# Kernel tuning notes

Hardware: AMD Instinct MI355X
Metric: run time of the kernel (lower is better)

The kernel has to match this reference:

```python
import jax, jax.numpy as jnp
import numpy as np

CLASS_NUM = 4            # number of positive classes
NUM_CLASSES = CLASS_NUM + 1  # last column is the negative class
W_P = 4.0
EPS = 1e-9
THR = 0.5


def setup_inputs() -> dict:
    key = jax.random.key(0)
    k1, k2 = jax.random.split(key)
    N = 4_000_000
    x = jax.random.normal(k1, (N, NUM_CLASSES), dtype=jnp.float32)
    t = jax.random.randint(k2, (N,), 0, NUM_CLASSES)
    return {"x": x, "t": t}


def _conf_mpu_loss(x, t):
    N = x.shape[0]
    p = jax.nn.softmax(x, axis=1)                       # [N, C]
    log_pneg = jnp.log(p[:, -1] + EPS)                  # [N]

    ones = jnp.ones((N,), dtype=jnp.float32)
    counts = jax.ops.segment_sum(ones, t, num_segments=NUM_CLASSES)  # per-class counts
    prior = counts[:CLASS_NUM] / N                      # empirical priors (positive classes)

    # loss_per_class: sum over samples with t==c of -log(p[n,c]+eps)
    logp_t = jnp.log(jnp.take_along_axis(p, t[:, None], axis=1)[:, 0] + EPS)
    class_losses = jax.ops.segment_sum(-logp_t, t, num_segments=NUM_CLASSES)

    # loss_per_class_neg: sum over samples with t==i (i positive) of -log(p_neg+eps)
    loss_neg = jax.ops.segment_sum(-log_pneg, t, num_segments=NUM_CLASSES)[:CLASS_NUM]

    # conf_loss_per_class
    conf = []
    for i in range(CLASS_NUM):
        mask = (p[:, i] > THR) & (t == i)
        nsel = jnp.sum(mask.astype(jnp.float32))
        li = jnp.sum(jnp.where(mask, -log_pneg / p[:, i], 0.0))
        conf.append(li / jnp.maximum(nsel, 1.0))        # li==0 when nsel==0
    mask_n = jnp.all(p <= THR, axis=1) & (t == CLASS_NUM)
    li_n = jnp.sum(jnp.where(mask_n, -log_pneg, 0.0))
    conf_neg = li_n / jnp.maximum(counts[CLASS_NUM], 1.0)  # li_n==0 when no selection
    conf_pos = jnp.stack(conf)                          # [CLASS_NUM]

    denom = jnp.maximum(1.0, counts[:CLASS_NUM])
    risk1 = jnp.sum(prior * class_losses[:CLASS_NUM] / denom)
    risk2 = jnp.sum(prior * conf_pos)
    risk3 = jnp.sum(prior * loss_neg / denom)
    risk4 = conf_neg

    positive_risk = W_P * (risk1 + risk2 - risk3)
    positive_risk = jnp.where(positive_risk < 0, 0.0, positive_risk)
    return positive_risk + risk4


def reference(x, t):
    return _conf_mpu_loss(x, t)
```

## Files before the change

### kernel.cpp

```cpp
#include <hip/hip_runtime.h>

namespace {
constexpr int BLOCK = 256;
constexpr int ROWS_PER_TILE = 1024;
constexpr int NACC = 22;
constexpr float EPSF = 1e-9f;
constexpr float THRF = 0.5f;
constexpr float WPF = 4.0f;
}

__device__ __forceinline__ float wave_reduce(float v) {
#pragma unroll
    for (int o = 32; o > 0; o >>= 1) v += __shfl_down(v, o, 64);
    return v;
}

__global__ __launch_bounds__(BLOCK) void mpu_main(const float* __restrict__ x,
                                                  const int* __restrict__ t,
                                                  float* __restrict__ acc, int N) {
    __shared__ float lds[ROWS_PER_TILE * 5];
    __shared__ float red[BLOCK / 64][NACC];

    float a[NACC];
#pragma unroll
    for (int j = 0; j < NACC; ++j) a[j] = 0.0f;

    const int tid = threadIdx.x;
    const int numTiles = (N + ROWS_PER_TILE - 1) / ROWS_PER_TILE;

    for (int tile = blockIdx.x; tile < numTiles; tile += gridDim.x) {
        const long long rowBase = (long long)tile * ROWS_PER_TILE;
        const int rows = min(ROWS_PER_TILE, (int)((long long)N - rowBase));
        const int nFloats = rows * 5;
        const float* src = x + rowBase * 5;
        const int n4 = nFloats >> 2;
        const float4* src4 = reinterpret_cast<const float4*>(src);
        float4* dst4 = reinterpret_cast<float4*>(lds);
        for (int i = tid; i < n4; i += BLOCK) dst4[i] = src4[i];
        for (int i = (n4 << 2) + tid; i < nFloats; i += BLOCK) lds[i] = src[i];
        __syncthreads();

        for (int k = tid; k < rows; k += BLOCK) {
            const float x0 = lds[k * 5 + 0], x1 = lds[k * 5 + 1], x2 = lds[k * 5 + 2],
                        x3 = lds[k * 5 + 3], x4 = lds[k * 5 + 4];
            const int tc = t[rowBase + k];

            const float mx = fmaxf(fmaxf(fmaxf(x0, x1), fmaxf(x2, x3)), x4);
            const float e0 = __expf(x0 - mx), e1 = __expf(x1 - mx),
                        e2 = __expf(x2 - mx), e3 = __expf(x3 - mx),
                        e4 = __expf(x4 - mx);
            const float r = 1.0f / (e0 + e1 + e2 + e3 + e4);
            const float p0 = e0 * r, p1 = e1 * r, p2 = e2 * r, p3 = e3 * r, p4 = e4 * r;

            const float nln = -__logf(p4 + EPSF);
            const float pt = (tc == 0) ? p0 : (tc == 1) ? p1 : (tc == 2) ? p2
                           : (tc == 3) ? p3 : p4;
            const float nlt = -__logf(pt + EPSF);

            const bool is0 = (tc == 0), is1 = (tc == 1), is2 = (tc == 2),
                       is3 = (tc == 3), is4 = (tc == 4);

            a[0] += is0 ? 1.0f : 0.0f;
            a[1] += is1 ? 1.0f : 0.0f;
            a[2] += is2 ? 1.0f : 0.0f;
            a[3] += is3 ? 1.0f : 0.0f;
            a[4] += is4 ? 1.0f : 0.0f;
            a[5] += is0 ? nlt : 0.0f;
            a[6] += is1 ? nlt : 0.0f;
            a[7] += is2 ? nlt : 0.0f;
            a[8] += is3 ? nlt : 0.0f;
            a[9]  += is0 ? nln : 0.0f;
            a[10] += is1 ? nln : 0.0f;
            a[11] += is2 ? nln : 0.0f;
            a[12] += is3 ? nln : 0.0f;
            const bool sel = (pt > THRF);
            const float confv = sel ? (nln / pt) : 0.0f;
            const float confn = sel ? 1.0f : 0.0f;
            a[13] += is0 ? confv : 0.0f;
            a[14] += is1 ? confv : 0.0f;
            a[15] += is2 ? confv : 0.0f;
            a[16] += is3 ? confv : 0.0f;
            a[17] += is0 ? confn : 0.0f;
            a[18] += is1 ? confn : 0.0f;
            a[19] += is2 ? confn : 0.0f;
            a[20] += is3 ? confn : 0.0f;
            const bool alle = (p0 <= THRF) && (p1 <= THRF) && (p2 <= THRF) &&
                              (p3 <= THRF) && (p4 <= THRF);
            a[21] += (is4 && alle) ? nln : 0.0f;
        }
        __syncthreads();
    }

    const int wave = tid >> 6;
    const int lane = tid & 63;
#pragma unroll
    for (int j = 0; j < NACC; ++j) {
        const float v = wave_reduce(a[j]);
        if (lane == 0) red[wave][j] = v;
    }
    __syncthreads();
    if (tid < NACC) {
        float v = red[0][tid] + red[1][tid] + red[2][tid] + red[3][tid];
        atomicAdd(&acc[tid], v);
    }
}

__global__ void mpu_final(const float* __restrict__ acc, float* __restrict__ out, int N) {
    if (threadIdx.x == 0 && blockIdx.x == 0) {
        const float invN = 1.0f / (float)N;
        float risk1 = 0.0f, risk2 = 0.0f, risk3 = 0.0f;
#pragma unroll
        for (int i = 0; i < 4; ++i) {
            const float cnt = acc[i];
            const float prior = cnt * invN;
            const float denom = fmaxf(1.0f, cnt);
            risk1 += prior * acc[5 + i] / denom;
            risk2 += prior * (acc[13 + i] / fmaxf(acc[17 + i], 1.0f));
            risk3 += prior * acc[9 + i] / denom;
        }
        const float risk4 = acc[21] / fmaxf(acc[4], 1.0f);
        float pos = WPF * (risk1 + risk2 - risk3);
        if (pos < 0.0f) pos = 0.0f;
        out[0] = pos + risk4;
    }
}

extern "C" void kernel_launch(void* const* d_in, const int* in_sizes, int n_in,
                              void* d_out, int out_size, void* d_ws, size_t ws_size,
                              hipStream_t stream) {
    const float* x = (const float*)d_in[0];
    const int* t = (const int*)d_in[1];
    float* out = (float*)d_out;
    float* acc = (float*)d_ws;
    const int N = in_sizes[1];

    hipMemsetAsync(acc, 0, NACC * sizeof(float), stream);

    const int numTiles = (N + ROWS_PER_TILE - 1) / ROWS_PER_TILE;
    const int grid = numTiles < 1024 ? numTiles : 1024;
    mpu_main<<<grid, BLOCK, 0, stream>>>(x, t, acc, N);
    mpu_final<<<1, 64, 0, stream>>>(acc, out, N);
}
```

Baseline: 148.3 us.

## Load four rows per thread via float4 directly, drop LDS staging, use log-sum-exp

Removes the LDS staging tile and its barriers. Each thread now reads four rows (20 floats) as five float4 loads plus one int4 label load straight from global memory. The softmax maths is rewritten as log-sum-exp, so each row needs one log instead of two, and the probability threshold tests are done on the exponentials and their sum without dividing. The grid is raised to 2048 blocks. The trade-offs are higher register pressure from holding four rows per thread, strided uncoalesced float4 loads across threads, and dropping EPS, which slightly changes numerics for very small probabilities.

```diff
diff --git a/kernel.cpp b/kernel.cpp
--- a/kernel.cpp
+++ b/kernel.cpp
@@ -2,10 +2,8 @@
 
 namespace {
 constexpr int BLOCK = 256;
-constexpr int ROWS_PER_TILE = 1024;
+constexpr int GRID = 2048;
 constexpr int NACC = 22;
-constexpr float EPSF = 1e-9f;
-constexpr float THRF = 0.5f;
 constexpr float WPF = 4.0f;
 }
 
@@ -18,90 +16,93 @@
 __global__ __launch_bounds__(BLOCK) void mpu_main(const float* __restrict__ x,
                                                   const int* __restrict__ t,
                                                   float* __restrict__ acc, int N) {
-    __shared__ float lds[ROWS_PER_TILE * 5];
     __shared__ float red[BLOCK / 64][NACC];
 
     float a[NACC];
 #pragma unroll
     for (int j = 0; j < NACC; ++j) a[j] = 0.0f;
 
-    const int tid = threadIdx.x;
-    const int numTiles = (N + ROWS_PER_TILE - 1) / ROWS_PER_TILE;
+    auto process = [&](float x0, float x1, float x2, float x3, float x4, int tc) {
+        const float mx = fmaxf(fmaxf(fmaxf(x0, x1), fmaxf(x2, x3)), x4);
+        const float e0 = __expf(x0 - mx), e1 = __expf(x1 - mx),
+                    e2 = __expf(x2 - mx), e3 = __expf(x3 - mx),
+                    e4 = __expf(x4 - mx);
+        const float sum = ((e0 + e1) + (e2 + e3)) + e4;
+        const float base = mx + __logf(sum);
+        const float nln = base - x4;
+        const float xt = (tc == 0) ? x0 : (tc == 1) ? x1 : (tc == 2) ? x2
+                       : (tc == 3) ? x3 : x4;
+        const float et = (tc == 0) ? e0 : (tc == 1) ? e1 : (tc == 2) ? e2
+                       : (tc == 3) ? e3 : e4;
+        const float nlt = base - xt;
 
-    for (int tile = blockIdx.x; tile < numTiles; tile += gridDim.x) {
-        const long long rowBase = (long long)tile * ROWS_PER_TILE;
-        const int rows = min(ROWS_PER_TILE, (int)((long long)N - rowBase));
-        const int nFloats = rows * 5;
-        const float* src = x + rowBase * 5;
-        const int n4 = nFloats >> 2;
-        const float4* src4 = reinterpret_cast<const float4*>(src);
-        float4* dst4 = reinterpret_cast<float4*>(lds);
-        for (int i = tid; i < n4; i += BLOCK) dst4[i] = src4[i];
-        for (int i = (n4 << 2) + tid; i < nFloats; i += BLOCK) lds[i] = src[i];
-        __syncthreads();
+        const bool is0 = (tc == 0), is1 = (tc == 1), is2 = (tc == 2),
+                   is3 = (tc == 3), is4 = (tc == 4);
+        const bool sel = (et + et > sum);
+        const bool alle = (sum >= 2.0f);
+        const float confv = sel ? nln * sum * __builtin_amdgcn_rcpf(et) : 0.0f;
+        const float confn = sel ? 1.0f : 0.0f;
 
-        for (int k = tid; k < rows; k += BLOCK) {
-            const float x0 = lds[k * 5 + 0], x1 = lds[k * 5 + 1], x2 = lds[k * 5 + 2],
-                        x3 = lds[k * 5 + 3], x4 = lds[k * 5 + 4];
-            const int tc = t[rowBase + k];
+        a[0] += is0 ? 1.0f : 0.0f;
+        a[1] += is1 ? 1.0f : 0.0f;
+        a[2] += is2 ? 1.0f : 0.0f;
+        a[3] += is3 ? 1.0f : 0.0f;
+        a[4] += is4 ? 1.0f : 0.0f;
+        a[5] += is0 ? nlt : 0.0f;
+        a[6] += is1 ? nlt : 0.0f;
+        a[7] += is2 ? nlt : 0.0f;
+        a[8] += is3 ? nlt : 0.0f;
+        a[9]  += is0 ? nln : 0.0f;
+        a[10] += is1 ? nln : 0.0f;
+        a[11] += is2 ? nln : 0.0f;
+        a[12] += is3 ? nln : 0.0f;
+        a[13] += is0 ? confv : 0.0f;
+        a[14] += is1 ? confv : 0.0f;
+        a[15] += is2 ? confv : 0.0f;
+        a[16] += is3 ? confv : 0.0f;
+        a[17] += is0 ? confn : 0.0f;
+        a[18] += is1 ? confn : 0.0f;
+        a[19] += is2 ? confn : 0.0f;
+        a[20] += is3 ? confn : 0.0f;
+        a[21] += (is4 && alle) ? nln : 0.0f;
+    };
 
-            const float mx = fmaxf(fmaxf(fmaxf(x0, x1), fmaxf(x2, x3)), x4);
-            const float e0 = __expf(x0 - mx), e1 = __expf(x1 - mx),
-                        e2 = __expf(x2 - mx), e3 = __expf(x3 - mx),
-                        e4 = __expf(x4 - mx);
-            const float r = 1.0f / (e0 + e1 + e2 + e3 + e4);
-            const float p0 = e0 * r, p1 = e1 * r, p2 = e2 * r, p3 = e3 * r, p4 = e4 * r;
+    const int gid = blockIdx.x * BLOCK + threadIdx.x;
+    const int stride = gridDim.x * BLOCK;
+    const int nGroups = N >> 2;
+    const float4* xv = reinterpret_cast<const float4*>(x);
+    const int4* tv = reinterpret_cast<const int4*>(t);
 
-            const float nln = -__logf(p4 + EPSF);
-            const float pt = (tc == 0) ? p0 : (tc == 1) ? p1 : (tc == 2) ? p2
-                           : (tc == 3) ? p3 : p4;
-            const float nlt = -__logf(pt + EPSF);
-
-            const bool is0 = (tc == 0), is1 = (tc == 1), is2 = (tc == 2),
-                       is3 = (tc == 3), is4 = (tc == 4);
-
-            a[0] += is0 ? 1.0f : 0.0f;
-            a[1] += is1 ? 1.0f : 0.0f;
-            a[2] += is2 ? 1.0f : 0.0f;
-            a[3] += is3 ? 1.0f : 0.0f;
-            a[4] += is4 ? 1.0f : 0.0f;
-            a[5] += is0 ? nlt : 0.0f;
-            a[6] += is1 ? nlt : 0.0f;
-            a[7] += is2 ? nlt : 0.0f;
-            a[8] += is3 ? nlt : 0.0f;
-            a[9]  += is0 ? nln : 0.0f;
-            a[10] += is1 ? nln : 0.0f;
-            a[11] += is2 ? nln : 0.0f;
-            a[12] += is3 ? nln : 0.0f;
-            const bool sel = (pt > THRF);
-            const float confv = sel ? (nln / pt) : 0.0f;
-            const float confn = sel ? 1.0f : 0.0f;
-            a[13] += is0 ? confv : 0.0f;
-            a[14] += is1 ? confv : 0.0f;
-            a[15] += is2 ? confv : 0.0f;
-            a[16] += is3 ? confv : 0.0f;
-            a[17] += is0 ? confn : 0.0f;
-            a[18] += is1 ? confn : 0.0f;
-            a[19] += is2 ? confn : 0.0f;
-            a[20] += is3 ? confn : 0.0f;
-            const bool alle = (p0 <= THRF) && (p1 <= THRF) && (p2 <= THRF) &&
-                              (p3 <= THRF) && (p4 <= THRF);
-            a[21] += (is4 && alle) ? nln : 0.0f;
-        }
-        __syncthreads();
+    for (int g = gid; g < nGroups; g += stride) {
+        const float4 v0 = xv[g * 5 + 0];
+        const float4 v1 = xv[g * 5 + 1];
+        const float4 v2 = xv[g * 5 + 2];
+        const float4 v3 = xv[g * 5 + 3];
+        const float4 v4 = xv[g * 5 + 4];
+        const int4 tt = tv[g];
+        process(v0.x, v0.y, v0.z, v0.w, v1.x, tt.x);
+        process(v1.y, v1.z, v1.w, v2.x, v2.y, tt.y);
+        process(v2.z, v2.w, v3.x, v3.y, v3.z, tt.z);
+        process(v3.w, v4.x, v4.y, v4.z, v4.w, tt.w);
+    }
+    if (gid == 0) {
+        for (int k = nGroups * 4; k < N; ++k)
+            process(x[k * 5 + 0], x[k * 5 + 1], x[k * 5 + 2], x[k * 5 + 3],
+                    x[k * 5 + 4], t[k]);
     }
 
-    const int wave = tid >> 6;
-    const int lane = tid & 63;
+    const int wave = threadIdx.x >> 6;
+    const int lane = threadIdx.x & 63;
 #pragma unroll
     for (int j = 0; j < NACC; ++j) {
         const float v = wave_reduce(a[j]);
         if (lane == 0) red[wave][j] = v;
     }
     __syncthreads();
-    if (tid < NACC) {
-        float v = red[0][tid] + red[1][tid] + red[2][tid] + red[3][tid];
-        atomicAdd(&acc[tid], v);
+    if (threadIdx.x < NACC) {
+        const float v = red[0][threadIdx.x] + red[1][threadIdx.x] +
+                        red[2][threadIdx.x] + red[3][threadIdx.x];
+        atomicAdd(&acc[threadIdx.x], v);
     }
 }
 
@@ -136,8 +137,10 @@
 
     hipMemsetAsync(acc, 0, NACC * sizeof(float), stream);
 
-    const int numTiles = (N + ROWS_PER_TILE - 1) / ROWS_PER_TILE;
-    const int grid = numTiles < 1024 ? numTiles : 1024;
+    const int nGroups = N >> 2;
+    int grid = (nGroups + BLOCK - 1) / BLOCK;
+    if (grid > GRID) grid = GRID;
+    if (grid < 1) grid = 1;
     mpu_main<<<grid, BLOCK, 0, stream>>>(x, t, acc, N);
     mpu_final<<<1, 64, 0, stream>>>(acc, out, N);
 }
```

Measured after the change: 148.8 us. No clear change (+0.3%).
